# Kernel tuning notes

Measured on AMD Instinct MI355X. Metric: run time of the kernel, lower is better.

## Reference

```python
import jax, jax.numpy as jnp
import numpy as np

B, S, D, R = 4, 4096, 1024, 128
EPS_MAG = 1e-8
EPS_LN = 1e-5


def setup_inputs() -> dict:
    key = jax.random.key(0)
    ks = jax.random.split(key, 24)
    w = lambda k, shape, s=0.02: (jax.random.normal(k, shape, jnp.float32) * s)
    d = {}
    d["x"] = jax.random.normal(ks[0], (B, S, D), jnp.float32)
    d["W_dt_down"] = w(ks[1], (D, R))            # dt_proj_down (no bias)
    d["W_dt_up"] = w(ks[2], (R, D))
    d["b_dt_up"] = jnp.full((D,), -4.0, jnp.float32)  # nn.init.constant_(-4.0)
    d["W_gate"] = w(ks[3], (D, D)); d["b_gate"] = jnp.zeros((D,), jnp.float32)
    d["W_phi1"] = w(ks[4], (D, D)); d["b_phi1"] = jnp.zeros((D,), jnp.float32)
    d["W_phi2"] = w(ks[5], (D, D)); d["b_phi2"] = jnp.zeros((D,), jnp.float32)
    d["omega_base"] = jax.random.normal(ks[6], (D,), jnp.float32) * 0.1
    d["W_omega"] = w(ks[7], (D, D)); d["b_omega"] = jnp.zeros((D,), jnp.float32)
    d["W_mag"] = w(ks[8], (D, D)); d["b_mag"] = jnp.zeros((D,), jnp.float32)
    d["W_qoff"] = w(ks[9], (D, D)); d["b_qoff"] = jnp.zeros((D,), jnp.float32)
    d["ln_g"] = jnp.ones((2 * D,), jnp.float32); d["ln_b"] = jnp.zeros((2 * D,), jnp.float32)
    d["W_out1"] = w(ks[10], (2 * D, D)); d["b_out1"] = jnp.zeros((D,), jnp.float32)
    d["W_out2"] = w(ks[11], (D, D)); d["b_out2"] = jnp.zeros((D,), jnp.float32)
    return d


def _forward(x, W_dt_down, W_dt_up, b_dt_up, W_gate, b_gate, W_phi1, b_phi1,
             W_phi2, b_phi2, omega_base, W_omega, b_omega, W_mag, b_mag,
             W_qoff, b_qoff, ln_g, ln_b, W_out1, b_out1, W_out2, b_out2):
    h = x  # expand_factor == 1 -> in_proj is Identity
    # input-dependent delta (low-rank)
    dt = jax.nn.softplus((h @ W_dt_down) @ W_dt_up + b_dt_up)        # [B,S,D]
    select_gate = jax.nn.sigmoid(h @ W_gate + b_gate)
    omega = omega_base + (h @ W_omega + b_omega)
    omega_scaled = omega * dt * 0.01
    phi_init = jax.nn.gelu(h @ W_phi1 + b_phi1, approximate=False) @ W_phi2 + b_phi2
    phi = phi_init + jnp.cumsum(omega_scaled, axis=1)                # phase accumulation
    magnitude = jax.nn.sigmoid(h @ W_mag + b_mag) * 5.0
    content = select_gate * h * magnitude
    memory_real = jnp.cumsum(content * jnp.cos(phi), axis=1)
    memory_imag = jnp.cumsum(content * jnp.sin(phi), axis=1)
    acc_mag = jnp.cumsum(magnitude * select_gate, axis=1)
    sqrt_mag = jnp.sqrt(acc_mag + EPS_MAG)
    mr = memory_real / sqrt_mag
    mi = memory_imag / sqrt_mag
    # rotation-based retrieval
    phi_q = phi + (h @ W_qoff + b_qoff)
    cq, sq = jnp.cos(phi_q), jnp.sin(phi_q)
    retrieved_real = mr * cq + mi * sq
    retrieved_imag = mi * cq - mr * sq
    ctx = jnp.concatenate([retrieved_real, retrieved_imag], axis=-1)  # [B,S,2D]
    mu = jnp.mean(ctx, axis=-1, keepdims=True)
    var = jnp.mean((ctx - mu) ** 2, axis=-1, keepdims=True)
    ln = (ctx - mu) / jnp.sqrt(var + EPS_LN) * ln_g + ln_b
    out = jax.nn.gelu(ln @ W_out1 + b_out1, approximate=False) @ W_out2 + b_out2
    return x + out


def reference(x, W_dt_down, W_dt_up, b_dt_up, W_gate, b_gate, W_phi1, b_phi1,
              W_phi2, b_phi2, omega_base, W_omega, b_omega, W_mag, b_mag,
              W_qoff, b_qoff, ln_g, ln_b, W_out1, b_out1, W_out2, b_out2):
    return _forward(x, W_dt_down, W_dt_up, b_dt_up, W_gate, b_gate, W_phi1, b_phi1,
                    W_phi2, b_phi2, omega_base, W_omega, b_omega, W_mag, b_mag,
                    W_qoff, b_qoff, ln_g, ln_b, W_out1, b_out1, W_out2, b_out2)
```

## Files before the change

kernel.cpp:

```cpp
#include <hip/hip_runtime.h>


#define D_ 1024
#define S_ 4096
#define BH 2
#define MH (BH*S_)
#define CHUNK 64
#define NCH (S_/CHUNK)

typedef float f32x4 __attribute__((ext_vector_type(4)));
typedef __bf16 bf16x8 __attribute__((ext_vector_type(8)));
typedef short s16x8 __attribute__((ext_vector_type(8)));

typedef __attribute__((address_space(1))) void gvoid;
typedef __attribute__((address_space(3))) void lvoid;

__device__ __forceinline__ void g2l16(const void* g, void* l) {
  __builtin_amdgcn_global_load_lds((gvoid*)g, (lvoid*)l, 16, 0, 0);
}

__device__ __forceinline__ float bflo(unsigned int w){ union{unsigned int i; float f;} c; c.i = w<<16; return c.f; }
__device__ __forceinline__ float bfhi(unsigned int w){ union{unsigned int i; float f;} c; c.i = w & 0xFFFF0000u; return c.f; }
__device__ __forceinline__ unsigned short f2bf(float f){
  union{float f; unsigned int i;} c; c.f=f;
  unsigned int u = c.i + 0x7FFFu + ((c.i>>16)&1u);
  return (unsigned short)(u>>16);
}
__device__ __forceinline__ unsigned int pack2(float lo, float hi){
  return (unsigned int)f2bf(lo) | ((unsigned int)f2bf(hi)<<16);
}

__device__ __forceinline__ float sig_(float x){ return 1.f/(1.f+__expf(-x)); }
__device__ __forceinline__ float gelu_(float x){ return 0.5f*x*(1.f+erff(x*0.70710678118654752440f)); }
__device__ __forceinline__ float softplus_(float x){ return (x>0.f) ? x + log1pf(__expf(-x)) : log1pf(__expf(x)); }

template<int EPI>
__global__ __launch_bounds__(256)
void gemm128(const unsigned short* __restrict__ A, int lda,
             const unsigned short* __restrict__ Bt, int ldb,
             int K, int N,
             const float* __restrict__ bias,
             const float* __restrict__ extra,
             void* __restrict__ Cout)
{
  __shared__ unsigned short As[128*32];
  __shared__ unsigned short Bs[128*32];
  const int tid = threadIdx.x;
  const int m0 = blockIdx.x * 128;
  const int n0 = blockIdx.y * 128;
  const int lane = tid & 63;
  const int wv = tid >> 6;
  const int wr = wv >> 1, wc = wv & 1;
  const int fr = lane & 15, fg = lane >> 4;

  const int r0 = tid >> 2;
  const int r1 = (tid + 256) >> 2;
  const int k8 = (tid & 3) * 8;

  f32x4 acc[4][4];
#pragma unroll
  for (int i=0;i<4;i++)
#pragma unroll
    for (int j=0;j<4;j++)
#pragma unroll
      for (int q=0;q<4;q++) acc[i][j][q] = 0.f;

  for (int k0 = 0; k0 < K; k0 += 32) {
    __syncthreads();
    g2l16(A  + (size_t)(m0+r0)*lda + k0 + k8, As + (size_t)tid*8);
    g2l16(A  + (size_t)(m0+r1)*lda + k0 + k8, As + (size_t)(tid+256)*8);
    g2l16(Bt + (size_t)(n0+r0)*ldb + k0 + k8, Bs + (size_t)tid*8);
    g2l16(Bt + (size_t)(n0+r1)*ldb + k0 + k8, Bs + (size_t)(tid+256)*8);
    __syncthreads();

    s16x8 af[4], bfr[4];
#pragma unroll
    for (int mf=0; mf<4; mf++) af[mf]  = *(const s16x8*)&As[(wr*64 + mf*16 + fr)*32 + fg*8];
#pragma unroll
    for (int nf=0; nf<4; nf++) bfr[nf] = *(const s16x8*)&Bs[(wc*64 + nf*16 + fr)*32 + fg*8];
#pragma unroll
    for (int mf=0; mf<4; mf++)
#pragma unroll
      for (int nf=0; nf<4; nf++)
        acc[mf][nf] = __builtin_amdgcn_mfma_f32_16x16x32_bf16(
          __builtin_bit_cast(bf16x8, af[mf]), __builtin_bit_cast(bf16x8, bfr[nf]),
          acc[mf][nf], 0, 0, 0);
  }

#pragma unroll
  for (int mf=0; mf<4; mf++) {
#pragma unroll
    for (int nf=0; nf<4; nf++) {
      const int gn = n0 + wc*64 + nf*16 + fr;
      float bv = 0.f;
      if constexpr (EPI != 5) bv = bias[gn];
#pragma unroll
      for (int q=0; q<4; q++) {
        const int gm = m0 + wr*64 + mf*16 + fg*4 + q;
        const size_t idx = (size_t)gm * N + gn;
        const float z = acc[mf][nf][q] + bv;
        if constexpr      (EPI == 0) ((unsigned short*)Cout)[idx] = f2bf(sig_(z));
        else if constexpr (EPI == 1) ((unsigned short*)Cout)[idx] = f2bf(z + extra[gn]);
        else if constexpr (EPI == 2) ((unsigned short*)Cout)[idx] = f2bf(gelu_(z));
        else if constexpr (EPI == 3) ((unsigned short*)Cout)[idx] = f2bf(sig_(z)*5.f);
        else if constexpr (EPI == 4) ((unsigned short*)Cout)[idx] = f2bf(z);
        else if constexpr (EPI == 5) ((unsigned short*)Cout)[idx] = f2bf(z);
        else if constexpr (EPI == 6) ((unsigned short*)Cout)[idx] = f2bf(softplus_(z));
        else                         ((float*)Cout)[idx]          = z + extra[idx];
      }
    }
  }
}

__global__ __launch_bounds__(256)
void cvtx_k(const float* __restrict__ x, unsigned int* __restrict__ hb)
{
  const size_t i = (size_t)blockIdx.x*256 + threadIdx.x;
  const float4 v = *(const float4*)(x + i*4);
  hb[i*2]   = pack2(v.x, v.y);
  hb[i*2+1] = pack2(v.z, v.w);
}

__global__ __launch_bounds__(256)
void tconv_k(const float* __restrict__ W, unsigned short* __restrict__ Wt, int K, int N)
{
  __shared__ float tile[32][33];
  const int kb = blockIdx.x*32, nb = blockIdx.y*32;
  const int tx = threadIdx.x & 31, ty = threadIdx.x >> 5;
#pragma unroll
  for (int i=0;i<32;i+=8) tile[ty+i][tx] = W[(size_t)(kb+ty+i)*N + (nb+tx)];
  __syncthreads();
#pragma unroll
  for (int i=0;i<32;i+=8) Wt[(size_t)(nb+ty+i)*K + (kb+tx)] = f2bf(tile[tx][ty+i]);
}

__global__ __launch_bounds__(256)
void scan1_k(unsigned int* __restrict__ zgate, unsigned int* __restrict__ zmag,
             unsigned int* __restrict__ zomega, const unsigned int* __restrict__ zdt,
             const unsigned int* __restrict__ hb,
             float* __restrict__ sumPhi, float* __restrict__ sumGm)
{
  const int flat = blockIdx.x*256 + threadIdx.x;
  const int dh = flat & 511;
  const int bc = flat >> 9;
  size_t i = (size_t)bc*CHUNK*(D_/2) + dh;
  float sp0=0,sp1=0,sg0=0,sg1=0;
  for (int s=0;s<CHUNK;s++,i+=D_/2) {
    const unsigned ga=zgate[i], mg=zmag[i], om=zomega[i], dt=zdt[i], hh=hb[i];
    const float ga0=bflo(ga), ga1=bfhi(ga), mg0=bflo(mg), mg1=bfhi(mg);
    const float od0 = bflo(om)*bflo(dt)*0.01f, od1 = bfhi(om)*bfhi(dt)*0.01f;
    const unsigned odp = pack2(od0, od1);
    zomega[i] = odp;
    sp0 += bflo(odp); sp1 += bfhi(odp);
    const float g0 = ga0*mg0, g1 = ga1*mg1;
    const unsigned gmp = pack2(g0, g1);
    zmag[i] = gmp;
    sg0 += bflo(gmp); sg1 += bfhi(gmp);
    zgate[i] = pack2(g0*bflo(hh), g1*bfhi(hh));
  }
  const int sidx = bc*D_ + dh*2;
  sumPhi[sidx]=sp0; sumPhi[sidx+1]=sp1;
  sumGm[sidx]=sg0;  sumGm[sidx+1]=sg1;
}

__global__ __launch_bounds__(256)
void scan2_k(float* __restrict__ a, float* __restrict__ b)
{
  const int ch = blockIdx.x*256 + threadIdx.x;
  const int bb = ch >> 10, d = ch & 1023;
  float r0=0.f, r1=0.f;
  for (int c=0;c<NCH;c++) {
    const size_t i = (size_t)(bb*NCH + c)*D_ + d;
    const float t=a[i]; a[i]=r0; r0+=t;
    const float u=b[i]; b[i]=r1; r1+=u;
  }
}

__global__ __launch_bounds__(256)
void scan3_k(const unsigned int* __restrict__ omdt, const unsigned int* __restrict__ content,
             const unsigned int* __restrict__ phinit, const float* __restrict__ phiOff,
             float* __restrict__ sumRe, float* __restrict__ sumIm)
{
  const int flat = blockIdx.x*256 + threadIdx.x;
  const int dh = flat & 511;
  const int bc = flat >> 9;
  size_t i = (size_t)bc*CHUNK*(D_/2) + dh;
  const int sidx = bc*D_ + dh*2;
  float p0 = phiOff[sidx], p1 = phiOff[sidx+1];
  float re0=0,re1=0,im0=0,im1=0;
  for (int s=0;s<CHUNK;s++,i+=D_/2) {
    const unsigned od = omdt[i], ct = content[i], pi = phinit[i];
    p0 += bflo(od); p1 += bfhi(od);
    const float phi0 = bflo(pi)+p0, phi1 = bfhi(pi)+p1;
    float s0,c0,s1,c1;
    __sincosf(phi0,&s0,&c0);
    __sincosf(phi1,&s1,&c1);
    const float ct0=bflo(ct), ct1=bfhi(ct);
    re0 += ct0*c0; im0 += ct0*s0;
    re1 += ct1*c1; im1 += ct1*s1;
  }
  sumRe[sidx]=re0; sumRe[sidx+1]=re1;
  sumIm[sidx]=im0; sumIm[sidx+1]=im1;
}

__global__ __launch_bounds__(256)
void scan5_k(const unsigned int* __restrict__ omdt, const unsigned int* __restrict__ content,
             const unsigned int* __restrict__ phinit, const unsigned int* __restrict__ gm,
             const unsigned int* __restrict__ qoff,
             const float* __restrict__ phiOff, const float* __restrict__ gmOff,
             const float* __restrict__ reOff, const float* __restrict__ imOff,
             unsigned int* __restrict__ ctx)
{
  const int flat = blockIdx.x*256 + threadIdx.x;
  const int dh = flat & 511;
  const int bc = flat >> 9;
  size_t i = (size_t)bc*CHUNK*(D_/2) + dh;
  const int sidx = bc*D_ + dh*2;
  float p0 = phiOff[sidx], p1 = phiOff[sidx+1];
  float ag0 = gmOff[sidx], ag1 = gmOff[sidx+1];
  float re0 = reOff[sidx], re1 = reOff[sidx+1];
  float im0 = imOff[sidx], im1 = imOff[sidx+1];
  const int mtok0 = bc*CHUNK;
  for (int s=0;s<CHUNK;s++,i+=D_/2) {
    const unsigned od = omdt[i], ct = content[i], pi = phinit[i], gq = gm[i], qo = qoff[i];
    p0 += bflo(od); p1 += bfhi(od);
    const float phi0 = bflo(pi)+p0, phi1 = bfhi(pi)+p1;
    float sn0,cs0,sn1,cs1;
    __sincosf(phi0,&sn0,&cs0);
    __sincosf(phi1,&sn1,&cs1);
    const float ct0=bflo(ct), ct1=bfhi(ct);
    re0 += ct0*cs0; im0 += ct0*sn0;
    re1 += ct1*cs1; im1 += ct1*sn1;
    ag0 += bflo(gq); ag1 += bfhi(gq);
    const float inv0 = rsqrtf(ag0 + 1e-8f), inv1 = rsqrtf(ag1 + 1e-8f);
    const float mr0 = re0*inv0, mi0 = im0*inv0;
    const float mr1 = re1*inv1, mi1 = im1*inv1;
    const float pq0 = phi0 + bflo(qo), pq1 = phi1 + bfhi(qo);
    float sq0,cq0,sq1,cq1;
    __sincosf(pq0,&sq0,&cq0);
    __sincosf(pq1,&sq1,&cq1);
    const size_t cb = (size_t)(mtok0+s)*D_ + dh;
    ctx[cb]        = pack2(mr0*cq0 + mi0*sq0, mr1*cq1 + mi1*sq1);
    ctx[cb + D_/2] = pack2(mi0*cq0 - mr0*sq0, mi1*cq1 - mr1*sq1);
  }
}

__global__ __launch_bounds__(256)
void ln_k(unsigned int* __restrict__ ctx, const float* __restrict__ gam, const float* __restrict__ bet)
{
  const int m = blockIdx.x, tid = threadIdx.x;
  const size_t base = (size_t)m*1024 + tid*4;
  const uint4 t = *(const uint4*)(ctx + base);
  float v[8] = { bflo(t.x), bfhi(t.x), bflo(t.y), bfhi(t.y),
                 bflo(t.z), bfhi(t.z), bflo(t.w), bfhi(t.w) };
  float s=0.f, ss=0.f;
#pragma unroll
  for (int j=0;j<8;j++){ s+=v[j]; ss+=v[j]*v[j]; }
  for (int o=32;o;o>>=1){ s += __shfl_xor(s,o); ss += __shfl_xor(ss,o); }
  __shared__ float red[8];
  const int wv = tid>>6, lane = tid&63;
  if (lane==0){ red[wv]=s; red[4+wv]=ss; }
  __syncthreads();
  s  = red[0]+red[1]+red[2]+red[3];
  ss = red[4]+red[5]+red[6]+red[7];
  const float mu = s*(1.f/2048.f);
  const float rstd = rsqrtf(ss*(1.f/2048.f) - mu*mu + 1e-5f);
  const int col = tid*8;
  float o[8];
#pragma unroll
  for (int j=0;j<8;j++) o[j] = (v[j]-mu)*rstd*gam[col+j] + bet[col+j];
  uint4 w;
  w.x = pack2(o[0],o[1]); w.y = pack2(o[2],o[3]);
  w.z = pack2(o[4],o[5]); w.w = pack2(o[6],o[7]);
  *(uint4*)(ctx + base) = w;
}

extern "C" void kernel_launch(void* const* d_in, const int* in_sizes, int n_in,
                              void* d_out, int out_size, void* d_ws, size_t ws_size,
                              hipStream_t stream)
{
  const float* x     = (const float*)d_in[0];
  const float* Wdd   = (const float*)d_in[1];
  const float* Wdu   = (const float*)d_in[2];
  const float* bdu   = (const float*)d_in[3];
  const float* Wg    = (const float*)d_in[4];
  const float* bg    = (const float*)d_in[5];
  const float* Wp1   = (const float*)d_in[6];
  const float* bp1   = (const float*)d_in[7];
  const float* Wp2   = (const float*)d_in[8];
  const float* bp2   = (const float*)d_in[9];
  const float* obase = (const float*)d_in[10];
  const float* Wo    = (const float*)d_in[11];
  const float* bo    = (const float*)d_in[12];
  const float* Wm    = (const float*)d_in[13];
  const float* bm    = (const float*)d_in[14];
  const float* Wq    = (const float*)d_in[15];
  const float* bq    = (const float*)d_in[16];
  const float* lng   = (const float*)d_in[17];
  const float* lnb   = (const float*)d_in[18];
  const float* Wo1   = (const float*)d_in[19];
  const float* bo1   = (const float*)d_in[20];
  const float* Wo2   = (const float*)d_in[21];
  const float* bo2   = (const float*)d_in[22];

  char* basep = (char*)d_ws;
  size_t off = 0;
  auto alloc = [&](size_t n) { char* q = basep + off; off = (off + n + 255) & ~(size_t)255; return q; };

  const size_t HZ = (size_t)MH*D_*2;
  unsigned short* hb    = (unsigned short*)alloc(HZ);
  unsigned short* zdt   = (unsigned short*)alloc(HZ);
  unsigned short* ctx   = hb;
  unsigned short* zgate = (unsigned short*)alloc(HZ);
  unsigned short* zomega= (unsigned short*)alloc(HZ);
  unsigned short* zmag  = (unsigned short*)alloc(HZ);
  unsigned short* zqoff = (unsigned short*)alloc(HZ);
  unsigned short* zpin  = (unsigned short*)alloc(HZ);
  unsigned short* zphi1 = (unsigned short*)alloc(HZ);
  unsigned short* a3    = zphi1;
  unsigned short* t1    = (unsigned short*)alloc((size_t)MH*128*2);
  unsigned short* wt_g  = (unsigned short*)alloc(1024*1024*2);
  unsigned short* wt_o  = (unsigned short*)alloc(1024*1024*2);
  unsigned short* wt_p1 = (unsigned short*)alloc(1024*1024*2);
  unsigned short* wt_m  = (unsigned short*)alloc(1024*1024*2);
  unsigned short* wt_q  = (unsigned short*)alloc(1024*1024*2);
  unsigned short* wt_p2 = (unsigned short*)alloc(1024*1024*2);
  unsigned short* wt_o2 = (unsigned short*)alloc(1024*1024*2);
  unsigned short* wt_dd = (unsigned short*)alloc(128*1024*2);
  unsigned short* wt_du = (unsigned short*)alloc(1024*128*2);
  unsigned short* wt_o1 = (unsigned short*)alloc((size_t)1024*2048*2);
  float* sumPhi = (float*)alloc((size_t)BH*NCH*D_*4);
  float* sumGm  = (float*)alloc((size_t)BH*NCH*D_*4);
  float* sumRe  = (float*)alloc((size_t)BH*NCH*D_*4);
  float* sumIm  = (float*)alloc((size_t)BH*NCH*D_*4);

  const dim3 blk(256);

  tconv_k<<<dim3(32,32), blk, 0, stream>>>(Wg,  wt_g,  1024,1024);
  tconv_k<<<dim3(32,32), blk, 0, stream>>>(Wo,  wt_o,  1024,1024);
  tconv_k<<<dim3(32,32), blk, 0, stream>>>(Wp1, wt_p1, 1024,1024);
  tconv_k<<<dim3(32,32), blk, 0, stream>>>(Wm,  wt_m,  1024,1024);
  tconv_k<<<dim3(32,32), blk, 0, stream>>>(Wq,  wt_q,  1024,1024);
  tconv_k<<<dim3(32,32), blk, 0, stream>>>(Wp2, wt_p2, 1024,1024);
  tconv_k<<<dim3(32,32), blk, 0, stream>>>(Wo2, wt_o2, 1024,1024);
  tconv_k<<<dim3(32,4),  blk, 0, stream>>>(Wdd, wt_dd, 1024,128);
  tconv_k<<<dim3(4,32),  blk, 0, stream>>>(Wdu, wt_du, 128,1024);
  tconv_k<<<dim3(64,32), blk, 0, stream>>>(Wo1, wt_o1, 2048,1024);

  for (int h = 0; h < 2; h++) {
    const float* xh  = x + (size_t)h*MH*D_;
    float* outh      = (float*)d_out + (size_t)h*MH*D_;

    cvtx_k<<<MH*D_/1024, blk, 0, stream>>>(xh, (unsigned int*)hb);

    const dim3 g8(MH/128, 8), g1(MH/128, 1);
    gemm128<2><<<g8, blk, 0, stream>>>(hb,1024,    wt_p1,1024, 1024,1024, bp1, nullptr, zphi1);
    gemm128<4><<<g8, blk, 0, stream>>>(zphi1,1024, wt_p2,1024, 1024,1024, bp2, nullptr, zpin);
    gemm128<0><<<g8, blk, 0, stream>>>(hb,1024,    wt_g,1024,  1024,1024, bg,  nullptr, zgate);
    gemm128<1><<<g8, blk, 0, stream>>>(hb,1024,    wt_o,1024,  1024,1024, bo,  obase,   zomega);
    gemm128<3><<<g8, blk, 0, stream>>>(hb,1024,    wt_m,1024,  1024,1024, bm,  nullptr, zmag);
    gemm128<4><<<g8, blk, 0, stream>>>(hb,1024,    wt_q,1024,  1024,1024, bq,  nullptr, zqoff);
    gemm128<5><<<g1, blk, 0, stream>>>(hb,1024,    wt_dd,1024, 1024,128,  nullptr,nullptr, t1);
    gemm128<6><<<g8, blk, 0, stream>>>(t1,128,     wt_du,128,  128,1024,  bdu, nullptr, zdt);

    scan1_k<<<256, blk, 0, stream>>>((unsigned int*)zgate,(unsigned int*)zmag,(unsigned int*)zomega,
                                     (const unsigned int*)zdt,(const unsigned int*)hb, sumPhi, sumGm);
    scan2_k<<<8, blk, 0, stream>>>(sumPhi, sumGm);
    scan3_k<<<256, blk, 0, stream>>>((const unsigned int*)zomega,(const unsigned int*)zgate,
                                     (const unsigned int*)zpin, sumPhi, sumRe, sumIm);
    scan2_k<<<8, blk, 0, stream>>>(sumRe, sumIm);
    scan5_k<<<256, blk, 0, stream>>>((const unsigned int*)zomega,(const unsigned int*)zgate,
                                     (const unsigned int*)zpin,(const unsigned int*)zmag,
                                     (const unsigned int*)zqoff,
                                     sumPhi, sumGm, sumRe, sumIm, (unsigned int*)ctx);

    ln_k<<<MH, blk, 0, stream>>>((unsigned int*)ctx, lng, lnb);
    gemm128<2><<<g8, blk, 0, stream>>>(ctx,2048, wt_o1,2048, 2048,1024, bo1, nullptr, a3);
    gemm128<7><<<g8, blk, 0, stream>>>(a3,1024,  wt_o2,1024, 1024,1024, bo2, xh, (float*)outh);
  }
}
```

Measured before the change: 901.6 us.

## Fuse input projections into one wide GEMM, batch output GEMMs, parallelize chunk scan

Concatenates the gate, omega, phi1, mag, qoff and dt-down weights into one 5248-wide weight so a single GEMM launch produces all input projections, with slice-dependent epilogues. The phi2 and dt-up GEMMs are merged into one launch. The scan and projection stages now run per sequence (4 chunks of 4096 rows), while LayerNorm and the two output GEMMs run once over all 16384 rows instead of per half. The serial carry scan over chunk sums is replaced by a wave-level shuffle prefix scan, and the weight conversions are batched into one kernel. The aim is fewer launches, better GPU fill for the wide GEMMs, and less serial scan latency, at the cost of a larger context buffer and more epilogue branching.

```diff
diff --git a/kernel.cpp b/kernel.cpp
--- a/kernel.cpp
+++ b/kernel.cpp
@@ -3,8 +3,8 @@
 
 #define D_ 1024
 #define S_ 4096
-#define BH 2
-#define MH (BH*S_)
+#define MQ 4096
+#define MF 16384
 #define CHUNK 64
 #define NCH (S_/CHUNK)
 
@@ -34,14 +34,18 @@
 __device__ __forceinline__ float gelu_(float x){ return 0.5f*x*(1.f+erff(x*0.70710678118654752440f)); }
 __device__ __forceinline__ float softplus_(float x){ return (x>0.f) ? x + log1pf(__expf(-x)) : log1pf(__expf(x)); }
 
-template<int EPI>
-__global__ __launch_bounds__(256)
-void gemm128(const unsigned short* __restrict__ A, int lda,
-             const unsigned short* __restrict__ Bt, int ldb,
-             int K, int N,
-             const float* __restrict__ bias,
-             const float* __restrict__ extra,
-             void* __restrict__ Cout)
+template<int MODE>
+__global__ __launch_bounds__(256)
+void gemmF(const unsigned short* __restrict__ A0,
+           const unsigned short* __restrict__ A1,
+           const unsigned short* __restrict__ B0,
+           const unsigned short* __restrict__ B1,
+           const float* __restrict__ bias0,
+           const float* __restrict__ bias1,
+           const float* __restrict__ extra,
+           unsigned short* __restrict__ out0,
+           unsigned short* __restrict__ out1,
+           float* __restrict__ outf)
 {
   __shared__ unsigned short As[128*32];
   __shared__ unsigned short Bs[128*32];
@@ -57,6 +61,16 @@
   const int r1 = (tid + 256) >> 2;
   const int k8 = (tid & 3) * 8;
 
+  const unsigned short* Ap; const unsigned short* Bp;
+  int lda, ldb, K, brow0;
+  if constexpr (MODE == 0)      { Ap=A0; lda=1024; K=1024; Bp=B0; ldb=1024; brow0=n0; }
+  else if constexpr (MODE == 2) { Ap=A0; lda=2048; K=2048; Bp=B0; ldb=2048; brow0=n0; }
+  else if constexpr (MODE == 3) { Ap=A0; lda=1024; K=1024; Bp=B0; ldb=1024; brow0=n0; }
+  else {
+    if (n0 < 1024) { Ap=A0; lda=1024; K=1024; Bp=B0; ldb=1024; brow0=n0; }
+    else           { Ap=A1; lda=128;  K=128;  Bp=B1; ldb=128;  brow0=n0-1024; }
+  }
+
   f32x4 acc[4][4];
 #pragma unroll
   for (int i=0;i<4;i++)
@@ -67,10 +81,10 @@
 
   for (int k0 = 0; k0 < K; k0 += 32) {
     __syncthreads();
-    g2l16(A  + (size_t)(m0+r0)*lda + k0 + k8, As + (size_t)tid*8);
-    g2l16(A  + (size_t)(m0+r1)*lda + k0 + k8, As + (size_t)(tid+256)*8);
-    g2l16(Bt + (size_t)(n0+r0)*ldb + k0 + k8, Bs + (size_t)tid*8);
-    g2l16(Bt + (size_t)(n0+r1)*ldb + k0 + k8, Bs + (size_t)(tid+256)*8);
+    g2l16(Ap + (size_t)(m0+r0)*lda + k0 + k8, As + (size_t)tid*8);
+    g2l16(Ap + (size_t)(m0+r1)*lda + k0 + k8, As + (size_t)(tid+256)*8);
+    g2l16(Bp + (size_t)(brow0+r0)*ldb + k0 + k8, Bs + (size_t)tid*8);
+    g2l16(Bp + (size_t)(brow0+r1)*ldb + k0 + k8, Bs + (size_t)(tid+256)*8);
     __syncthreads();
 
     s16x8 af[4], bfr[4];
@@ -87,26 +101,37 @@
           acc[mf][nf], 0, 0, 0);
   }
 
+  const int slice = n0 >> 10;
 #pragma unroll
   for (int mf=0; mf<4; mf++) {
 #pragma unroll
     for (int nf=0; nf<4; nf++) {
       const int gn = n0 + wc*64 + nf*16 + fr;
-      float bv = 0.f;
-      if constexpr (EPI != 5) bv = bias[gn];
+      float bv;
+      if constexpr (MODE == 1) bv = (n0 < 1024) ? bias0[gn] : bias1[gn-1024];
+      else bv = bias0[gn];
 #pragma unroll
       for (int q=0; q<4; q++) {
         const int gm = m0 + wr*64 + mf*16 + fg*4 + q;
-        const size_t idx = (size_t)gm * N + gn;
         const float z = acc[mf][nf][q] + bv;
-        if constexpr      (EPI == 0) ((unsigned short*)Cout)[idx] = f2bf(sig_(z));
-        else if constexpr (EPI == 1) ((unsigned short*)Cout)[idx] = f2bf(z + extra[gn]);
-        else if constexpr (EPI == 2) ((unsigned short*)Cout)[idx] = f2bf(gelu_(z));
-        else if constexpr (EPI == 3) ((unsigned short*)Cout)[idx] = f2bf(sig_(z)*5.f);
-        else if constexpr (EPI == 4) ((unsigned short*)Cout)[idx] = f2bf(z);
-        else if constexpr (EPI == 5) ((unsigned short*)Cout)[idx] = f2bf(z);
-        else if constexpr (EPI == 6) ((unsigned short*)Cout)[idx] = f2bf(softplus_(z));
-        else                         ((float*)Cout)[idx]          = z + extra[idx];
+        if constexpr (MODE == 0) {
+          if (slice < 5) {
+            const float r = (slice==0) ? sig_(z)
+                          : (slice==2) ? gelu_(z)
+                          : (slice==3) ? sig_(z)*5.f : z;
+            out0[(size_t)slice*MQ*1024 + (size_t)gm*1024 + (gn&1023)] = f2bf(r);
+          } else {
+            out1[(size_t)gm*128 + (gn-5120)] = f2bf(z);
+          }
+        } else if constexpr (MODE == 1) {
+          if (slice == 0) out0[(size_t)gm*1024 + gn] = f2bf(z);
+          else            out1[(size_t)gm*1024 + (gn-1024)] = f2bf(softplus_(z));
+        } else if constexpr (MODE == 2) {
+          out0[(size_t)gm*1024 + gn] = f2bf(gelu_(z));
+        } else {
+          const size_t idx = (size_t)gm*1024 + gn;
+          outf[idx] = z + extra[idx];
+        }
       }
     }
   }
@@ -132,6 +157,39 @@
   __syncthreads();
 #pragma unroll
   for (int i=0;i<32;i+=8) Wt[(size_t)(nb+ty+i)*K + (kb+tx)] = f2bf(tile[tx][ty+i]);
+}
+
+struct P7 { const float* s[7]; unsigned short* d[7]; };
+__global__ __launch_bounds__(256)
+void tconv7_k(P7 p)
+{
+  __shared__ float tile[32][33];
+  const float* W = p.s[blockIdx.z];
+  unsigned short* Wt = p.d[blockIdx.z];
+  const int kb = blockIdx.x*32, nb = blockIdx.y*32;
+  const int tx = threadIdx.x & 31, ty = threadIdx.x >> 5;
+#pragma unroll
+  for (int i=0;i<32;i+=8) tile[ty+i][tx] = W[(size_t)(kb+ty+i)*1024 + (nb+tx)];
+  __syncthreads();
+#pragma unroll
+  for (int i=0;i<32;i+=8) Wt[(size_t)(nb+ty+i)*1024 + (kb+tx)] = f2bf(tile[tx][ty+i]);
+}
+
+__global__ __launch_bounds__(256)
+void biascat_k(const float* bg, const float* bo, const float* ob, const float* bp1,
+               const float* bm, const float* bq, float* bc)
+{
+  const int i = blockIdx.x*256 + threadIdx.x;
+  if (i >= 5248) return;
+  const int s = i >> 10, d = i & 1023;
+  float v;
+  if (s==0) v = bg[d];
+  else if (s==1) v = bo[d] + ob[d];
+  else if (s==2) v = bp1[d];
+  else if (s==3) v = bm[d];
+  else if (s==4) v = bq[d];
+  else v = 0.f;
+  bc[i] = v;
 }
 
 __global__ __launch_bounds__(256)
@@ -166,14 +224,19 @@
 __global__ __launch_bounds__(256)
 void scan2_k(float* __restrict__ a, float* __restrict__ b)
 {
-  const int ch = blockIdx.x*256 + threadIdx.x;
-  const int bb = ch >> 10, d = ch & 1023;
-  float r0=0.f, r1=0.f;
-  for (int c=0;c<NCH;c++) {
-    const size_t i = (size_t)(bb*NCH + c)*D_ + d;
-    const float t=a[i]; a[i]=r0; r0+=t;
-    const float u=b[i]; b[i]=r1; r1+=u;
-  }
+  const int chain = (blockIdx.x*256 + threadIdx.x) >> 6;
+  const int lane  = threadIdx.x & 63;
+  const size_t i = (size_t)lane*D_ + chain;
+  const float v = a[i], w = b[i];
+  float vi = v, wi = w;
+#pragma unroll
+  for (int off=1; off<64; off<<=1) {
+    const float t = __shfl_up(vi, off, 64);
+    const float u = __shfl_up(wi, off, 64);
+    if (lane >= off) { vi += t; wi += u; }
+  }
+  a[i] = vi - v;
+  b[i] = wi - w;
 }
 
 __global__ __launch_bounds__(256)
@@ -307,75 +370,78 @@
   size_t off = 0;
   auto alloc = [&](size_t n) { char* q = basep + off; off = (off + n + 255) & ~(size_t)255; return q; };
 
-  const size_t HZ = (size_t)MH*D_*2;
-  unsigned short* hb    = (unsigned short*)alloc(HZ);
-  unsigned short* zdt   = (unsigned short*)alloc(HZ);
-  unsigned short* ctx   = hb;
-  unsigned short* zgate = (unsigned short*)alloc(HZ);
-  unsigned short* zomega= (unsigned short*)alloc(HZ);
-  unsigned short* zmag  = (unsigned short*)alloc(HZ);
-  unsigned short* zqoff = (unsigned short*)alloc(HZ);
-  unsigned short* zpin  = (unsigned short*)alloc(HZ);
-  unsigned short* zphi1 = (unsigned short*)alloc(HZ);
-  unsigned short* a3    = zphi1;
-  unsigned short* t1    = (unsigned short*)alloc((size_t)MH*128*2);
-  unsigned short* wt_g  = (unsigned short*)alloc(1024*1024*2);
-  unsigned short* wt_o  = (unsigned short*)alloc(1024*1024*2);
-  unsigned short* wt_p1 = (unsigned short*)alloc(1024*1024*2);
-  unsigned short* wt_m  = (unsigned short*)alloc(1024*1024*2);
-  unsigned short* wt_q  = (unsigned short*)alloc(1024*1024*2);
-  unsigned short* wt_p2 = (unsigned short*)alloc(1024*1024*2);
-  unsigned short* wt_o2 = (unsigned short*)alloc(1024*1024*2);
-  unsigned short* wt_dd = (unsigned short*)alloc(128*1024*2);
-  unsigned short* wt_du = (unsigned short*)alloc(1024*128*2);
-  unsigned short* wt_o1 = (unsigned short*)alloc((size_t)1024*2048*2);
-  float* sumPhi = (float*)alloc((size_t)BH*NCH*D_*4);
-  float* sumGm  = (float*)alloc((size_t)BH*NCH*D_*4);
-  float* sumRe  = (float*)alloc((size_t)BH*NCH*D_*4);
-  float* sumIm  = (float*)alloc((size_t)BH*NCH*D_*4);
+  unsigned short* ctxF = (unsigned short*)alloc((size_t)MF*2048*2);
+  char* qbase = alloc((size_t)5*MQ*1024*2 + (size_t)2*MQ*1024*2
+                      + (size_t)MQ*1024*2 + (size_t)MQ*128*2);
+  unsigned short* cat1 = (unsigned short*)qbase;
+  unsigned short* cat2 = cat1 + (size_t)5*MQ*1024;
+  unsigned short* hb   = cat2 + (size_t)2*MQ*1024;
+  unsigned short* t1   = hb   + (size_t)MQ*1024;
+  unsigned short* a3   = (unsigned short*)qbase;
+  unsigned short* wt_cat = (unsigned short*)alloc((size_t)5248*1024*2);
+  unsigned short* wt_p2  = (unsigned short*)alloc(1024*1024*2);
+  unsigned short* wt_du  = (unsigned short*)alloc(1024*128*2);
+  unsigned short* wt_o1  = (unsigned short*)alloc((size_t)1024*2048*2);
+  unsigned short* wt_o2  = (unsigned short*)alloc(1024*1024*2);
+  float* bias_cat = (float*)alloc(5248*4);
+  float* sumPhi = (float*)alloc((size_t)NCH*D_*4);
+  float* sumGm  = (float*)alloc((size_t)NCH*D_*4);
+  float* sumRe  = (float*)alloc((size_t)NCH*D_*4);
+  float* sumIm  = (float*)alloc((size_t)NCH*D_*4);
 
   const dim3 blk(256);
 
-  tconv_k<<<dim3(32,32), blk, 0, stream>>>(Wg,  wt_g,  1024,1024);
-  tconv_k<<<dim3(32,32), blk, 0, stream>>>(Wo,  wt_o,  1024,1024);
-  tconv_k<<<dim3(32,32), blk, 0, stream>>>(Wp1, wt_p1, 1024,1024);
-  tconv_k<<<dim3(32,32), blk, 0, stream>>>(Wm,  wt_m,  1024,1024);
-  tconv_k<<<dim3(32,32), blk, 0, stream>>>(Wq,  wt_q,  1024,1024);
-  tconv_k<<<dim3(32,32), blk, 0, stream>>>(Wp2, wt_p2, 1024,1024);
-  tconv_k<<<dim3(32,32), blk, 0, stream>>>(Wo2, wt_o2, 1024,1024);
-  tconv_k<<<dim3(32,4),  blk, 0, stream>>>(Wdd, wt_dd, 1024,128);
+  P7 p7;
+  p7.s[0]=Wg;  p7.d[0]=wt_cat + (size_t)0*1024*1024;
+  p7.s[1]=Wo;  p7.d[1]=wt_cat + (size_t)1*1024*1024;
+  p7.s[2]=Wp1; p7.d[2]=wt_cat + (size_t)2*1024*1024;
+  p7.s[3]=Wm;  p7.d[3]=wt_cat + (size_t)3*1024*1024;
+  p7.s[4]=Wq;  p7.d[4]=wt_cat + (size_t)4*1024*1024;
+  p7.s[5]=Wp2; p7.d[5]=wt_p2;
+  p7.s[6]=Wo2; p7.d[6]=wt_o2;
+  tconv7_k<<<dim3(32,32,7), blk, 0, stream>>>(p7);
+  tconv_k<<<dim3(32,4),  blk, 0, stream>>>(Wdd, wt_cat + (size_t)5120*1024, 1024,128);
   tconv_k<<<dim3(4,32),  blk, 0, stream>>>(Wdu, wt_du, 128,1024);
   tconv_k<<<dim3(64,32), blk, 0, stream>>>(Wo1, wt_o1, 2048,1024);
-
-  for (int h = 0; h < 2; h++) {
-    const float* xh  = x + (size_t)h*MH*D_;
-    float* outh      = (float*)d_out + (size_t)h*MH*D_;
-
-    cvtx_k<<<MH*D_/1024, blk, 0, stream>>>(xh, (unsigned int*)hb);
-
-    const dim3 g8(MH/128, 8), g1(MH/128, 1);
-    gemm128<2><<<g8, blk, 0, stream>>>(hb,1024,    wt_p1,1024, 1024,1024, bp1, nullptr, zphi1);
-    gemm128<4><<<g8, blk, 0, stream>>>(zphi1,1024, wt_p2,1024, 1024,1024, bp2, nullptr, zpin);
-    gemm128<0><<<g8, blk, 0, stream>>>(hb,1024,    wt_g,1024,  1024,1024, bg,  nullptr, zgate);
-    gemm128<1><<<g8, blk, 0, stream>>>(hb,1024,    wt_o,1024,  1024,1024, bo,  obase,   zomega);
-    gemm128<3><<<g8, blk, 0, stream>>>(hb,1024,    wt_m,1024,  1024,1024, bm,  nullptr, zmag);
-    gemm128<4><<<g8, blk, 0, stream>>>(hb,1024,    wt_q,1024,  1024,1024, bq,  nullptr, zqoff);
-    gemm128<5><<<g1, blk, 0, stream>>>(hb,1024,    wt_dd,1024, 1024,128,  nullptr,nullptr, t1);
-    gemm128<6><<<g8, blk, 0, stream>>>(t1,128,     wt_du,128,  128,1024,  bdu, nullptr, zdt);
-
-    scan1_k<<<256, blk, 0, stream>>>((unsigned int*)zgate,(unsigned int*)zmag,(unsigned int*)zomega,
+  biascat_k<<<21, blk, 0, stream>>>(bg, bo, obase, bp1, bm, bq, bias_cat);
+
+  unsigned short* zgate  = cat1;
+  unsigned short* zomega = cat1 + (size_t)1*MQ*1024;
+  unsigned short* zphi1  = cat1 + (size_t)2*MQ*1024;
+  unsigned short* zmag   = cat1 + (size_t)3*MQ*1024;
+  unsigned short* zqoff  = cat1 + (size_t)4*MQ*1024;
+  unsigned short* zpin   = cat2;
+  unsigned short* zdt    = cat2 + (size_t)1*MQ*1024;
+
+  for (int q = 0; q < 4; q++) {
+    const float* xq = x + (size_t)q*MQ*D_;
+
+    cvtx_k<<<MQ*D_/1024, blk, 0, stream>>>(xq, (unsigned int*)hb);
+
+    gemmF<0><<<dim3(MQ/128, 41), blk, 0, stream>>>(hb, nullptr, wt_cat, nullptr,
+                                                   bias_cat, nullptr, nullptr,
+                                                   cat1, t1, nullptr);
+    gemmF<1><<<dim3(MQ/128, 16), blk, 0, stream>>>(zphi1, t1, wt_p2, wt_du,
+                                                   bp2, bdu, nullptr,
+                                                   zpin, zdt, nullptr);
+    scan1_k<<<128, blk, 0, stream>>>((unsigned int*)zgate,(unsigned int*)zmag,(unsigned int*)zomega,
                                      (const unsigned int*)zdt,(const unsigned int*)hb, sumPhi, sumGm);
-    scan2_k<<<8, blk, 0, stream>>>(sumPhi, sumGm);
-    scan3_k<<<256, blk, 0, stream>>>((const unsigned int*)zomega,(const unsigned int*)zgate,
+    scan2_k<<<256, blk, 0, stream>>>(sumPhi, sumGm);
+    scan3_k<<<128, blk, 0, stream>>>((const unsigned int*)zomega,(const unsigned int*)zgate,
                                      (const unsigned int*)zpin, sumPhi, sumRe, sumIm);
-    scan2_k<<<8, blk, 0, stream>>>(sumRe, sumIm);
-    scan5_k<<<256, blk, 0, stream>>>((const unsigned int*)zomega,(const unsigned int*)zgate,
+    scan2_k<<<256, blk, 0, stream>>>(sumRe, sumIm);
+    scan5_k<<<128, blk, 0, stream>>>((const unsigned int*)zomega,(const unsigned int*)zgate,
                                      (const unsigned int*)zpin,(const unsigned int*)zmag,
                                      (const unsigned int*)zqoff,
-                                     sumPhi, sumGm, sumRe, sumIm, (unsigned int*)ctx);
-
-    ln_k<<<MH, blk, 0, stream>>>((unsigned int*)ctx, lng, lnb);
-    gemm128<2><<<g8, blk, 0, stream>>>(ctx,2048, wt_o1,2048, 2048,1024, bo1, nullptr, a3);
-    gemm128<7><<<g8, blk, 0, stream>>>(a3,1024,  wt_o2,1024, 1024,1024, bo2, xh, (float*)outh);
-  }
-}
+                                     sumPhi, sumGm, sumRe, sumIm,
+                                     (unsigned int*)ctxF + (size_t)q*MQ*1024);
+  }
+
+  ln_k<<<MF, blk, 0, stream>>>((unsigned int*)ctxF, lng, lnb);
+  gemmF<2><<<dim3(MF/128, 8), blk, 0, stream>>>(ctxF, nullptr, wt_o1, nullptr,
+                                                bo1, nullptr, nullptr,
+                                                a3, nullptr, nullptr);
+  gemmF<3><<<dim3(MF/128, 8), blk, 0, stream>>>(a3, nullptr, wt_o2, nullptr,
+                                                bo2, nullptr, x,
+                                                nullptr, nullptr, (float*)d_out);
+}
```

Result: slower. 931.5 us (+3.3%).
